# Optimization experiments

Measured on AMD Instinct MI355X. Metric: run time of the kernel, lower is better.

The kernel has to match this reference:

```python
import jax, jax.numpy as jnp
import numpy as np

B, S, H, N, L = 256, 64, 512, 16, 2
OUT_BITS = 32            # ceil(log2(n)), n = 2**32
PTR_BITS = 6             # ceil(log2(seq_len)), seq_len = 64
OUT_DIM = 3 + PTR_BITS   # = 9
T = 2 * OUT_BITS - 1     # 63 sequential decode steps


def _ln(x, g, b):
    m = jnp.mean(x, -1, keepdims=True)
    v = jnp.mean((x - m) ** 2, -1, keepdims=True)
    return (x - m) * jax.lax.rsqrt(v + 1e-5) * g + b


def _s4_step(A, Bm, Cm, D, oW, ob, s, x):
    # diagonal-SSM S4 block step: s (B,H,N) recurrent state, x (B,H) input
    s2 = A * s + Bm * x[:, :, None]
    y = jnp.einsum('bhn,hn->bh', s2, Cm) + D * x
    y = jax.nn.gelu(y, approximate=False) @ oW + ob
    return s2, y


def _forward(input_seq, in_W, in_b, A, Bm, Cm, D, outW, outb, ln_g, ln_b, head_W, head_b):
    Bsz = input_seq.shape[0]
    dt = input_seq.dtype
    x = input_seq @ in_W + in_b            # (B,S,H)
    encoded = x                            # encoded_inputs saved before S4 stack
    # ---- encoder: L S4 blocks, residual + layernorm ----
    for j in range(L):
        def step(s, xt, j=j):
            return _s4_step(A[j], Bm[j], Cm[j], D[j], outW[j], outb[j], s, xt)
        s0 = jnp.zeros((Bsz, H, N), dt)
        _, ys = jax.lax.scan(step, s0, jnp.swapaxes(x, 0, 1))
        x = _ln(jnp.swapaxes(ys, 0, 1) + x, ln_g[j], ln_b[j])
    dec0 = jnp.broadcast_to(jnp.array([0.0, 0.0, 1.0], dt), (Bsz, 3))
    carry0 = (jnp.zeros((L, Bsz, H, N), dt), jnp.zeros((Bsz, H), dt), dec0)
    ones1 = jnp.ones((Bsz, 1), dt)

    def dstep(carry, i):
        states, ctx, dec_in = carry
        dp = dec_in @ in_W + in_b          # (B,H)
        xd = dp
        new_states = []
        for j in range(L):
            s2, y = _s4_step(A[j], Bm[j], Cm[j], D[j], outW[j], outb[j], states[j], xd)
            new_states.append(s2)
            res = jnp.where(i == 0, dp, y)   # torch code: residual=proj on step 0, else doubles x_dec
            xd = _ln(y + res, ln_g[j], ln_b[j])
        is_out = (i % 2) == 0
        # pointer retrieval (only applied on odd steps via where)
        o_ptr = jax.nn.sigmoid((xd + ctx) @ head_W + head_b)
        ptr = jnp.argmax(o_ptr[:, 3:3 + PTR_BITS], axis=1)            # (B,)
        ptr_vec = jnp.take_along_axis(encoded, ptr[:, None, None], axis=1)[:, 0]
        ctx = jnp.where(is_out, ctx, ctx + ptr_vec)
        out = jax.nn.sigmoid((xd + ctx) @ head_W + head_b)            # (B,OUT_DIM)
        next_char = jnp.where(is_out, (out[:, 0:1] > 0.5).astype(dt), jnp.zeros((Bsz, 1), dt))
        tag0 = jnp.where(is_out, 1.0, 0.0) * ones1
        tag1 = ones1 - tag0
        dec_next = jnp.concatenate([next_char, tag0, tag1], axis=1)   # (B,3)
        return (jnp.stack(new_states), ctx, dec_next), out

    _, outs = jax.lax.scan(dstep, carry0, jnp.arange(T))
    return jnp.swapaxes(outs, 0, 1)        # (B, T, OUT_DIM)


def setup_inputs() -> dict:
    ks = jax.random.split(jax.random.key(0), 8)
    f32 = jnp.float32
    return {
        'input_seq': jax.random.uniform(ks[0], (B, S, 3), f32),
        'autoregressive_steps': T,
        'in_W': jax.random.normal(ks[1], (3, H), f32) * 0.5,
        'in_b': jnp.zeros((H,), f32),
        'A': jax.random.uniform(ks[2], (L, H, N), f32, 0.5, 0.99),
        'Bm': jax.random.normal(ks[3], (L, H, N), f32) * 0.1,
        'Cm': jax.random.normal(ks[4], (L, H, N), f32) * 0.1,
        'D': jnp.ones((L, H), f32),
        'outW': jax.random.normal(ks[5], (L, H, H), f32) * 0.02,
        'outb': jnp.zeros((L, H), f32),
        'ln_g': jnp.ones((L, H), f32),
        'ln_b': jnp.zeros((L, H), f32),
        'head_W': jax.random.normal(ks[6], (H, OUT_DIM), f32) * 0.05,
        'head_b': jnp.zeros((OUT_DIM,), f32),
    }


def reference(input_seq, autoregressive_steps, in_W, in_b, A, Bm, Cm, D, outW, outb, ln_g, ln_b, head_W, head_b):
    return _forward(input_seq, in_W, in_b, A, Bm, Cm, D, outW, outb, ln_g, ln_b, head_W, head_b)
```

## Files before the change

kernel.cpp:

```cpp
#include <hip/hip_runtime.h>
#include <math.h>

#define HDIM   512
#define NDIM   16
#define SEQ    64
#define TSTEPS 63
#define BATCH  256
#define ODIM   9
#define NTHR   512


__device__ __forceinline__ float gelu_f32(float x) {
    return 0.5f * x * (1.0f + erff(x * 0.70710678118654752440f));
}

__device__ __forceinline__ float sig32(float x) {
    return 1.0f / (1.0f + expf(-x));
}

__device__ __forceinline__ void load3_l2(const float* p0, const float* p1,
                                         const float* p2,
                                         float& v0, float& v1, float& v2) {
    asm volatile(
        "global_load_dword %0, %3, off sc0\n\t"
        "global_load_dword %1, %4, off sc0\n\t"
        "global_load_dword %2, %5, off sc0\n\t"
        "s_waitcnt vmcnt(0)"
        : "=&v"(v0), "=&v"(v1), "=&v"(v2)
        : "v"(p0), "v"(p1), "v"(p2)
        : "memory");
}
__device__ __forceinline__ float load1_l2(const float* p) {
    float v;
    asm volatile("global_load_dword %0, %1, off sc0\n\t"
                 "s_waitcnt vmcnt(0)"
                 : "=v"(v) : "v"(p) : "memory");
    return v;
}

__global__ __launch_bounds__(NTHR, 2)
void s4_decode_kernel(
    const float* __restrict__ input_seq,
    const float* __restrict__ in_W,
    const float* __restrict__ in_b,
    const float* __restrict__ Aarr,
    const float* __restrict__ Barr,
    const float* __restrict__ Carr,
    const float* __restrict__ Darr,
    const float* __restrict__ outW,
    const float* __restrict__ outb,
    const float* __restrict__ ln_g,
    const float* __restrict__ ln_b,
    const float* __restrict__ headW,
    const float* __restrict__ headb,
    float* __restrict__ out,
    float* gws, float* zws,
    unsigned* fg, unsigned* fz,
    unsigned* fx, unsigned* xid)
{
    __shared__ float  ld_xd[HDIM];
    __shared__ float  ld_gall[4 * HDIM];
    __shared__ float4 ld_z4[16 * 4 * 32];
    __shared__ float  ld_D0[HDIM];
    __shared__ float  ld_D1[HDIM];
    __shared__ float  ld_red[16];
    __shared__ float  ld_hred[8 * ODIM];
    __shared__ float  ld_logit[ODIM + 1];
    __shared__ float  ld_dec[4];
    __shared__ int    ld_ptr;
    __shared__ int    ld_fast;

    const int b    = blockIdx.x;
    const int tid  = threadIdx.x;
    const int hg   = tid >> 4;
    const int n    = tid & 15;
    const int mem  = (b >> 3) & 3;
    const int gbase = b - 8 * mem;
    const int c4   = tid & 31;
    const int rg   = tid >> 5;
    const int rgE  = (rg + ((b * 5) & 15)) & 15;
    const int base_row = rgE * 32;
    const int j0 = 0 + (0 >= mem), j1 = 1 + (1 >= mem), j2 = 2 + (2 >= mem);

    unsigned myxcd;
    asm volatile("s_getreg_b32 %0, hwreg(HW_REG_XCC_ID)" : "=s"(myxcd));
    if (tid == 0) {
        __hip_atomic_store(&xid[b], myxcd, __ATOMIC_RELAXED, __HIP_MEMORY_SCOPE_AGENT);
        __hip_atomic_store(&fx[b], 1u, __ATOMIC_RELEASE, __HIP_MEMORY_SCOPE_AGENT);
        unsigned ok = 1;
        #pragma unroll
        for (int j = 0; j < 4; ++j) {
            if (j == mem) continue;
            while (__hip_atomic_load(&fx[gbase + 8 * j],
                                     __ATOMIC_ACQUIRE, __HIP_MEMORY_SCOPE_AGENT) == 0)
                __builtin_amdgcn_s_sleep(1);
            ok &= (__hip_atomic_load(&xid[gbase + 8 * j],
                                     __ATOMIC_RELAXED, __HIP_MEMORY_SCOPE_AGENT) == myxcd);
        }
        ld_fast = (int)ok;
    }

    float s0[16], s1[16];
    float A0[16], B0[16], C0[16], A1[16], B1[16], C1[16];
    #pragma unroll
    for (int k = 0; k < 16; ++k) {
        int h  = hg + 32 * k;
        int i0 = h * NDIM + n;
        int i1 = (HDIM + h) * NDIM + n;
        A0[k] = Aarr[i0]; B0[k] = Barr[i0]; C0[k] = Carr[i0];
        A1[k] = Aarr[i1]; B1[k] = Barr[i1]; C1[k] = Carr[i1];
        s0[k] = 0.f; s1[k] = 0.f;
    }

    const float inb_t = in_b[tid];
    const float w0 = in_W[tid], w1 = in_W[HDIM + tid], w2 = in_W[2 * HDIM + tid];
    const float ob0 = outb[tid], ob1 = outb[HDIM + tid];
    const float lg0 = ln_g[tid], lg1 = ln_g[HDIM + tid];
    const float lb0 = ln_b[tid], lb1 = ln_b[HDIM + tid];

    ld_D0[tid] = Darr[tid];
    ld_D1[tid] = Darr[HDIM + tid];

    const float4* Wsl = (const float4*)outW + mem * 32 + c4;

    float ctxr = 0.f;
    if (tid == 0) { ld_dec[0] = 0.f; ld_dec[1] = 0.f; ld_dec[2] = 1.f; }
    __syncthreads();
    const bool fast = (ld_fast != 0);

    for (int i = 0; i < TSTEPS; ++i) {
        float dpv = fmaf(ld_dec[0], w0, fmaf(ld_dec[1], w1, fmaf(ld_dec[2], w2, inb_t)));
        __syncthreads();
        ld_xd[tid] = dpv;
        __syncthreads();

        #pragma unroll 1
        for (int blk = 0; blk < 2; ++blk) {
            const unsigned seq = (unsigned)(2 * i + blk + 1);
            {
                float* s  = blk ? s1 : s0;
                float* Ar = blk ? A1 : A0;
                float* Br = blk ? B1 : B0;
                float* Cr = blk ? C1 : C0;
                const float* Dl = blk ? ld_D1 : ld_D0;
                #pragma unroll
                for (int k = 0; k < 16; ++k) {
                    int h = hg + 32 * k;
                    float xh = ld_xd[h];
                    float sv = fmaf(Ar[k], s[k], Br[k] * xh);
                    s[k] = sv;
                    float p = sv * Cr[k];
                    p += __shfl_xor(p, 1);
                    p += __shfl_xor(p, 2);
                    p += __shfl_xor(p, 4);
                    p += __shfl_xor(p, 8);
                    if (n == 0) ld_gall[mem * HDIM + h] = gelu_f32(p + Dl[h] * xh);
                }
            }
            __syncthreads();
            if (fast) {
                gws[b * HDIM + tid] = ld_gall[mem * HDIM + tid];
            } else {
                __hip_atomic_store(&gws[b * HDIM + tid], ld_gall[mem * HDIM + tid],
                                   __ATOMIC_RELAXED, __HIP_MEMORY_SCOPE_AGENT);
            }
            __syncthreads();
            if (tid == 4)
                __hip_atomic_store(&fg[b], seq, __ATOMIC_RELAXED, __HIP_MEMORY_SCOPE_AGENT);
            if (tid < 3) {
                int j = tid + (tid >= mem ? 1 : 0);
                while (__hip_atomic_load(&fg[gbase + 8 * j],
                                         __ATOMIC_RELAXED, __HIP_MEMORY_SCOPE_AGENT) < seq)
                    __builtin_amdgcn_s_sleep(1);
            }
            __syncthreads();
            if (fast) {
                float v0, v1, v2;
                load3_l2(&gws[(gbase + 8 * j0) * HDIM + tid],
                         &gws[(gbase + 8 * j1) * HDIM + tid],
                         &gws[(gbase + 8 * j2) * HDIM + tid], v0, v1, v2);
                ld_gall[j0 * HDIM + tid] = v0;
                ld_gall[j1 * HDIM + tid] = v1;
                ld_gall[j2 * HDIM + tid] = v2;
            } else {
                ld_gall[j0 * HDIM + tid] =
                    __hip_atomic_load(&gws[(gbase + 8 * j0) * HDIM + tid],
                                      __ATOMIC_RELAXED, __HIP_MEMORY_SCOPE_AGENT);
                ld_gall[j1 * HDIM + tid] =
                    __hip_atomic_load(&gws[(gbase + 8 * j1) * HDIM + tid],
                                      __ATOMIC_RELAXED, __HIP_MEMORY_SCOPE_AGENT);
                ld_gall[j2 * HDIM + tid] =
                    __hip_atomic_load(&gws[(gbase + 8 * j2) * HDIM + tid],
                                      __ATOMIC_RELAXED, __HIP_MEMORY_SCOPE_AGENT);
            }
            __syncthreads();
            {
                const float4* Wb = Wsl + (size_t)blk * HDIM * 128;
                float4 acc[4];
                #pragma unroll
                for (int bi = 0; bi < 4; ++bi) acc[bi] = make_float4(0.f, 0.f, 0.f, 0.f);
                float4 a0 = Wb[(size_t)(base_row)     * 128];
                float4 a1 = Wb[(size_t)(base_row + 1) * 128];
                #pragma unroll 2
                for (int rr = 0; rr < 32; rr += 4) {
                    int rB = base_row + ((rr + 2) & 31);
                    float4 b0 = Wb[(size_t)rB * 128];
                    float4 b1 = Wb[(size_t)(rB + 1) * 128];
                    {
                        int r = base_row + rr;
                        #pragma unroll
                        for (int bi = 0; bi < 4; ++bi) {
                            float g0 = ld_gall[bi * HDIM + r];
                            float g1 = ld_gall[bi * HDIM + r + 1];
                            acc[bi].x = fmaf(g1, a1.x, fmaf(g0, a0.x, acc[bi].x));
                            acc[bi].y = fmaf(g1, a1.y, fmaf(g0, a0.y, acc[bi].y));
                            acc[bi].z = fmaf(g1, a1.z, fmaf(g0, a0.z, acc[bi].z));
                            acc[bi].w = fmaf(g1, a1.w, fmaf(g0, a0.w, acc[bi].w));
                        }
                    }
                    int rA = base_row + ((rr + 4) & 31);
                    a0 = Wb[(size_t)rA * 128];
                    a1 = Wb[(size_t)(rA + 1) * 128];
                    {
                        int r = base_row + rr + 2;
                        #pragma unroll
                        for (int bi = 0; bi < 4; ++bi) {
                            float g0 = ld_gall[bi * HDIM + r];
                            float g1 = ld_gall[bi * HDIM + r + 1];
                            acc[bi].x = fmaf(g1, b1.x, fmaf(g0, b0.x, acc[bi].x));
                            acc[bi].y = fmaf(g1, b1.y, fmaf(g0, b0.y, acc[bi].y));
                            acc[bi].z = fmaf(g1, b1.z, fmaf(g0, b0.z, acc[bi].z));
                            acc[bi].w = fmaf(g1, b1.w, fmaf(g0, b0.w, acc[bi].w));
                        }
                    }
                }
                #pragma unroll
                for (int bi = 0; bi < 4; ++bi)
                    ld_z4[(rg * 4 + bi) * 32 + c4] = acc[bi];
            }
            __syncthreads();
            {
                const float* zf = (const float*)ld_z4;
                int bi2 = tid >> 7;
                int col = tid & 127;
                float zv = 0.f;
                #pragma unroll
                for (int k = 0; k < 16; ++k) zv += zf[(k * 4 + bi2) * 128 + col];
                float* zp = &zws[(gbase + 8 * bi2) * HDIM + mem * 128 + col];
                if (fast) *zp = zv;
                else __hip_atomic_store(zp, zv, __ATOMIC_RELAXED, __HIP_MEMORY_SCOPE_AGENT);
            }
            __syncthreads();
            if (tid == 4)
                __hip_atomic_store(&fz[b], seq, __ATOMIC_RELAXED, __HIP_MEMORY_SCOPE_AGENT);
            if (tid < 3) {
                int j = tid + (tid >= mem ? 1 : 0);
                while (__hip_atomic_load(&fz[gbase + 8 * j],
                                         __ATOMIC_RELAXED, __HIP_MEMORY_SCOPE_AGENT) < seq)
                    __builtin_amdgcn_s_sleep(1);
            }
            __syncthreads();
            {
                float zraw = fast ? load1_l2(&zws[b * HDIM + tid])
                                  : __hip_atomic_load(&zws[b * HDIM + tid],
                                                      __ATOMIC_RELAXED,
                                                      __HIP_MEMORY_SCOPE_AGENT);
                float z = zraw + (blk ? ob1 : ob0);
                float res = (i == 0) ? dpv : z;
                float tmp = z + res;
                float v1 = tmp, v2 = tmp * tmp;
                #pragma unroll
                for (int m = 1; m < 64; m <<= 1) {
                    v1 += __shfl_xor(v1, m);
                    v2 += __shfl_xor(v2, m);
                }
                if ((tid & 63) == 0) {
                    ld_red[2 * (tid >> 6)]     = v1;
                    ld_red[2 * (tid >> 6) + 1] = v2;
                }
                __syncthreads();
                float s1r = 0.f, s2r = 0.f;
                #pragma unroll
                for (int q = 0; q < 8; ++q) { s1r += ld_red[2*q]; s2r += ld_red[2*q+1]; }
                float mu  = s1r * (1.f / 512.f);
                float var = s2r * (1.f / 512.f) - mu * mu;
                float rs  = rsqrtf(var + 1e-5f);
                __syncthreads();
                ld_xd[tid] = (tmp - mu) * rs * (blk ? lg1 : lg0) + (blk ? lb1 : lb0);
                __syncthreads();
            }
        }

        {
            float v = ld_xd[tid] + ctxr;
            const float* w = headW + tid * ODIM;
            float p[ODIM];
            #pragma unroll
            for (int o = 0; o < ODIM; ++o) p[o] = v * w[o];
            #pragma unroll
            for (int m = 1; m < 64; m <<= 1) {
                #pragma unroll
                for (int o = 0; o < ODIM; ++o) p[o] += __shfl_xor(p[o], m);
            }
            if ((tid & 63) == 0) {
                int wv = tid >> 6;
                #pragma unroll
                for (int o = 0; o < ODIM; ++o) ld_hred[wv * ODIM + o] = p[o];
            }
            __syncthreads();
            if (tid < ODIM) {
                float s = headb[tid];
                #pragma unroll
                for (int wv = 0; wv < 8; ++wv) s += ld_hred[wv * ODIM + tid];
                ld_logit[tid] = s;
            }
            __syncthreads();
        }

        const bool is_out = ((i & 1) == 0);
        if (is_out) {
            if (tid < ODIM)
                out[(b * TSTEPS + i) * ODIM + tid] = sig32(ld_logit[tid]);
            if (tid == 0) {
                float nc = (sig32(ld_logit[0]) > 0.5f) ? 1.f : 0.f;
                ld_dec[0] = nc; ld_dec[1] = 1.f; ld_dec[2] = 0.f;
            }
            __syncthreads();
        } else {
            if (tid == 0) {
                int best = 0; float bv = sig32(ld_logit[3]);
                #pragma unroll
                for (int o = 1; o < 6; ++o) {
                    float v2 = sig32(ld_logit[3 + o]);
                    if (v2 > bv) { bv = v2; best = o; }
                }
                ld_ptr = best;
                ld_dec[0] = 0.f; ld_dec[1] = 0.f; ld_dec[2] = 1.f;
            }
            __syncthreads();
            {
                const float* iseq = input_seq + (b * SEQ + ld_ptr) * 3;
                float e0 = iseq[0], e1 = iseq[1], e2 = iseq[2];
                ctxr += fmaf(e0, w0, fmaf(e1, w1, fmaf(e2, w2, inb_t)));
            }
            __syncthreads();
            {
                float v = ld_xd[tid] + ctxr;
                const float* w = headW + tid * ODIM;
                float p[ODIM];
                #pragma unroll
                for (int o = 0; o < ODIM; ++o) p[o] = v * w[o];
                #pragma unroll
                for (int m = 1; m < 64; m <<= 1) {
                    #pragma unroll
                    for (int o = 0; o < ODIM; ++o) p[o] += __shfl_xor(p[o], m);
                }
                if ((tid & 63) == 0) {
                    int wv = tid >> 6;
                    #pragma unroll
                    for (int o = 0; o < ODIM; ++o) ld_hred[wv * ODIM + o] = p[o];
                }
                __syncthreads();
                if (tid < ODIM) {
                    float s = headb[tid];
                    #pragma unroll
                    for (int wv = 0; wv < 8; ++wv) s += ld_hred[wv * ODIM + tid];
                    out[(b * TSTEPS + i) * ODIM + tid] = sig32(s);
                }
            }
            __syncthreads();
        }
    }
}

extern "C" void kernel_launch(void* const* d_in, const int* in_sizes, int n_in,
                              void* d_out, int out_size, void* d_ws, size_t ws_size,
                              hipStream_t stream) {
    (void)in_sizes; (void)n_in; (void)ws_size; (void)out_size;
    const float* input_seq = (const float*)d_in[0];
    const float* in_W   = (const float*)d_in[2];
    const float* in_b   = (const float*)d_in[3];
    const float* Aarr   = (const float*)d_in[4];
    const float* Barr   = (const float*)d_in[5];
    const float* Carr   = (const float*)d_in[6];
    const float* Darr   = (const float*)d_in[7];
    const float* outW   = (const float*)d_in[8];
    const float* outb   = (const float*)d_in[9];
    const float* ln_g   = (const float*)d_in[10];
    const float* ln_b   = (const float*)d_in[11];
    const float* headW  = (const float*)d_in[12];
    const float* headb  = (const float*)d_in[13];
    float* out = (float*)d_out;

    unsigned* fg  = (unsigned*)d_ws;
    unsigned* fz  = fg + BATCH;
    unsigned* fx  = fz + BATCH;
    unsigned* xid = fx + BATCH;
    float* gws = (float*)((char*)d_ws + 4096);
    float* zws = gws + BATCH * HDIM;

    hipMemsetAsync(d_ws, 0, 4096, stream);

    s4_decode_kernel<<<BATCH, NTHR, 0, stream>>>(
        input_seq, in_W, in_b, Aarr, Barr, Carr, Darr,
        outW, outb, ln_g, ln_b, headW, headb, out,
        gws, zws, fg, fz, fx, xid);
}
```

Before: 1.357 ms.

## Split hidden dim across 4-block groups so each block computes SSM for all 4 batches

Before, each block ran the full S4 recurrence for its own batch row and exchanged GELU outputs with the three peer blocks through global memory, then did a column-sliced matmul. Now each block owns a quarter of the hidden dimension for all four batch rows in its group. That removes the GELU exchange round (gws and fg flags) and leaves a single z-exchange per layer. The shuffle reduction is restructured as a transpose-style butterfly, the matmul uses float4 LDS reads with a 4-row prefetch, and head weights are cached in registers. The trade-offs are higher register pressure (launch bounds drop to 1 block per CU) and redundant layernorm and head work for all four rows in every block.

```diff
diff --git a/kernel.cpp b/kernel.cpp
--- a/kernel.cpp
+++ b/kernel.cpp
@@ -8,7 +8,11 @@
 #define BATCH  256
 #define ODIM   9
 #define NTHR   512
-
+#define GSTR   132
+#define SPIN_CAP (1 << 24)
+
+
+typedef float f32x4 __attribute__((ext_vector_type(4)));
 
 __device__ __forceinline__ float gelu_f32(float x) {
     return 0.5f * x * (1.0f + erff(x * 0.70710678118654752440f));
@@ -18,27 +22,30 @@
     return 1.0f / (1.0f + expf(-x));
 }
 
-__device__ __forceinline__ void load3_l2(const float* p0, const float* p1,
-                                         const float* p2,
-                                         float& v0, float& v1, float& v2) {
+__device__ __forceinline__ void load4x4_l2(const f32x4* p0, const f32x4* p1,
+                                           const f32x4* p2, const f32x4* p3,
+                                           f32x4& v0, f32x4& v1, f32x4& v2, f32x4& v3) {
     asm volatile(
-        "global_load_dword %0, %3, off sc0\n\t"
-        "global_load_dword %1, %4, off sc0\n\t"
-        "global_load_dword %2, %5, off sc0\n\t"
+        "global_load_dwordx4 %0, %4, off sc0\n\t"
+        "global_load_dwordx4 %1, %5, off sc0\n\t"
+        "global_load_dwordx4 %2, %6, off sc0\n\t"
+        "global_load_dwordx4 %3, %7, off sc0\n\t"
         "s_waitcnt vmcnt(0)"
-        : "=&v"(v0), "=&v"(v1), "=&v"(v2)
-        : "v"(p0), "v"(p1), "v"(p2)
+        : "=&v"(v0), "=&v"(v1), "=&v"(v2), "=&v"(v3)
+        : "v"(p0), "v"(p1), "v"(p2), "v"(p3)
         : "memory");
 }
-__device__ __forceinline__ float load1_l2(const float* p) {
-    float v;
-    asm volatile("global_load_dword %0, %1, off sc0\n\t"
-                 "s_waitcnt vmcnt(0)"
-                 : "=v"(v) : "v"(p) : "memory");
-    return v;
-}
-
-__global__ __launch_bounds__(NTHR, 2)
+
+__device__ __forceinline__ void fma_row4(float4& acc, const float4 g,
+                                         const float4 w0, const float4 w1,
+                                         const float4 w2, const float4 w3) {
+    acc.x = fmaf(g.w, w3.x, fmaf(g.z, w2.x, fmaf(g.y, w1.x, fmaf(g.x, w0.x, acc.x))));
+    acc.y = fmaf(g.w, w3.y, fmaf(g.z, w2.y, fmaf(g.y, w1.y, fmaf(g.x, w0.y, acc.y))));
+    acc.z = fmaf(g.w, w3.z, fmaf(g.z, w2.z, fmaf(g.y, w1.z, fmaf(g.x, w0.z, acc.z))));
+    acc.w = fmaf(g.w, w3.w, fmaf(g.z, w2.w, fmaf(g.y, w1.w, fmaf(g.x, w0.w, acc.w))));
+}
+
+__global__ __launch_bounds__(NTHR, 1)
 void s4_decode_kernel(
     const float* __restrict__ input_seq,
     const float* __restrict__ in_W,
@@ -54,33 +61,28 @@
     const float* __restrict__ headW,
     const float* __restrict__ headb,
     float* __restrict__ out,
-    float* gws, float* zws,
-    unsigned* fg, unsigned* fz,
+    float* zws,
+    unsigned* fz,
     unsigned* fx, unsigned* xid)
 {
-    __shared__ float  ld_xd[HDIM];
-    __shared__ float  ld_gall[4 * HDIM];
-    __shared__ float4 ld_z4[16 * 4 * 32];
-    __shared__ float  ld_D0[HDIM];
-    __shared__ float  ld_D1[HDIM];
-    __shared__ float  ld_red[16];
-    __shared__ float  ld_hred[8 * ODIM];
-    __shared__ float  ld_logit[ODIM + 1];
-    __shared__ float  ld_dec[4];
-    __shared__ int    ld_ptr;
+    __shared__ __align__(16) float  ld_x[4 * HDIM];
+    __shared__ __align__(16) float  ld_g[4 * GSTR];
+    __shared__ float4 ld_z4[16 * 128];
+    __shared__ float  ld_red[64];
+    __shared__ __align__(16) float  ld_hred[8 * 36];
+    __shared__ float  ld_logit[36];
+    __shared__ float  ld_dec[16];
+    __shared__ int    ld_ptr[4];
     __shared__ int    ld_fast;
 
-    const int b    = blockIdx.x;
-    const int tid  = threadIdx.x;
-    const int hg   = tid >> 4;
-    const int n    = tid & 15;
-    const int mem  = (b >> 3) & 3;
+    const int b     = blockIdx.x;
+    const int tid   = threadIdx.x;
+    const int n     = tid & 15;
+    const int hl32  = tid >> 4;
+    const int mem   = (b >> 3) & 3;
     const int gbase = b - 8 * mem;
-    const int c4   = tid & 31;
-    const int rg   = tid >> 5;
-    const int rgE  = (rg + ((b * 5) & 15)) & 15;
-    const int base_row = rgE * 32;
-    const int j0 = 0 + (0 >= mem), j1 = 1 + (1 >= mem), j2 = 2 + (2 >= mem);
+    const int hbase = 128 * mem;
+    const size_t zbase = (size_t)(((b >> 5) << 3) + (b & 7)) * (4 * HDIM * 4);
 
     unsigned myxcd;
     asm volatile("s_getreg_b32 %0, hwreg(HW_REG_XCC_ID)" : "=s"(myxcd));
@@ -91,9 +93,12 @@
         #pragma unroll
         for (int j = 0; j < 4; ++j) {
             if (j == mem) continue;
+            int guard = 0;
             while (__hip_atomic_load(&fx[gbase + 8 * j],
-                                     __ATOMIC_ACQUIRE, __HIP_MEMORY_SCOPE_AGENT) == 0)
+                                     __ATOMIC_ACQUIRE, __HIP_MEMORY_SCOPE_AGENT) == 0) {
                 __builtin_amdgcn_s_sleep(1);
+                if (++guard > SPIN_CAP) { ok = 0; break; }
+            }
             ok &= (__hip_atomic_load(&xid[gbase + 8 * j],
                                      __ATOMIC_RELAXED, __HIP_MEMORY_SCOPE_AGENT) == myxcd);
         }
@@ -101,217 +106,273 @@
     }
 
     float s0[16], s1[16];
-    float A0[16], B0[16], C0[16], A1[16], B1[16], C1[16];
+    float A0[4], B0[4], C0[4], A1[4], B1[4], C1[4], Dm0[4], Dm1[4];
     #pragma unroll
-    for (int k = 0; k < 16; ++k) {
-        int h  = hg + 32 * k;
-        int i0 = h * NDIM + n;
-        int i1 = (HDIM + h) * NDIM + n;
+    for (int k = 0; k < 4; ++k) {
+        const int h  = hbase + hl32 + 32 * k;
+        const int i0 = h * NDIM + n;
+        const int i1 = (HDIM + h) * NDIM + n;
         A0[k] = Aarr[i0]; B0[k] = Barr[i0]; C0[k] = Carr[i0];
         A1[k] = Aarr[i1]; B1[k] = Barr[i1]; C1[k] = Carr[i1];
-        s0[k] = 0.f; s1[k] = 0.f;
+        Dm0[k] = (n == 0) ? Darr[h] : 0.f;
+        Dm1[k] = (n == 0) ? Darr[HDIM + h] : 0.f;
     }
+    #pragma unroll
+    for (int v = 0; v < 16; ++v) { s0[v] = 0.f; s1[v] = 0.f; }
 
     const float inb_t = in_b[tid];
     const float w0 = in_W[tid], w1 = in_W[HDIM + tid], w2 = in_W[2 * HDIM + tid];
     const float ob0 = outb[tid], ob1 = outb[HDIM + tid];
     const float lg0 = ln_g[tid], lg1 = ln_g[HDIM + tid];
     const float lb0 = ln_b[tid], lb1 = ln_b[HDIM + tid];
-
-    ld_D0[tid] = Darr[tid];
-    ld_D1[tid] = Darr[HDIM + tid];
-
-    const float4* Wsl = (const float4*)outW + mem * 32 + c4;
-
-    float ctxr = 0.f;
-    if (tid == 0) { ld_dec[0] = 0.f; ld_dec[1] = 0.f; ld_dec[2] = 1.f; }
+    float hw[ODIM];
+    #pragma unroll
+    for (int o = 0; o < ODIM; ++o) hw[o] = headW[tid * ODIM + o];
+
+    float ctx[4] = {0.f, 0.f, 0.f, 0.f};
+    if (tid < 4) { ld_dec[4 * tid] = 0.f; ld_dec[4 * tid + 1] = 0.f; ld_dec[4 * tid + 2] = 1.f; }
     __syncthreads();
     const bool fast = (ld_fast != 0);
 
     for (int i = 0; i < TSTEPS; ++i) {
-        float dpv = fmaf(ld_dec[0], w0, fmaf(ld_dec[1], w1, fmaf(ld_dec[2], w2, inb_t)));
+        float dpr[4];
+        #pragma unroll
+        for (int j = 0; j < 4; ++j) {
+            dpr[j] = fmaf(ld_dec[4 * j], w0,
+                     fmaf(ld_dec[4 * j + 1], w1,
+                     fmaf(ld_dec[4 * j + 2], w2, inb_t)));
+            ld_x[j * HDIM + tid] = dpr[j];
+        }
         __syncthreads();
-        ld_xd[tid] = dpv;
-        __syncthreads();
-
-        #pragma unroll 1
+
+        float xn[4];
+
+        #pragma unroll
         for (int blk = 0; blk < 2; ++blk) {
             const unsigned seq = (unsigned)(2 * i + blk + 1);
-            {
-                float* s  = blk ? s1 : s0;
-                float* Ar = blk ? A1 : A0;
-                float* Br = blk ? B1 : B0;
-                float* Cr = blk ? C1 : C0;
-                const float* Dl = blk ? ld_D1 : ld_D0;
-                #pragma unroll
-                for (int k = 0; k < 16; ++k) {
-                    int h = hg + 32 * k;
-                    float xh = ld_xd[h];
-                    float sv = fmaf(Ar[k], s[k], Br[k] * xh);
-                    s[k] = sv;
-                    float p = sv * Cr[k];
-                    p += __shfl_xor(p, 1);
-                    p += __shfl_xor(p, 2);
-                    p += __shfl_xor(p, 4);
-                    p += __shfl_xor(p, 8);
-                    if (n == 0) ld_gall[mem * HDIM + h] = gelu_f32(p + Dl[h] * xh);
-                }
-            }
-            __syncthreads();
-            if (fast) {
-                gws[b * HDIM + tid] = ld_gall[mem * HDIM + tid];
-            } else {
-                __hip_atomic_store(&gws[b * HDIM + tid], ld_gall[mem * HDIM + tid],
-                                   __ATOMIC_RELAXED, __HIP_MEMORY_SCOPE_AGENT);
-            }
-            __syncthreads();
-            if (tid == 4)
-                __hip_atomic_store(&fg[b], seq, __ATOMIC_RELAXED, __HIP_MEMORY_SCOPE_AGENT);
-            if (tid < 3) {
-                int j = tid + (tid >= mem ? 1 : 0);
-                while (__hip_atomic_load(&fg[gbase + 8 * j],
-                                         __ATOMIC_RELAXED, __HIP_MEMORY_SCOPE_AGENT) < seq)
-                    __builtin_amdgcn_s_sleep(1);
-            }
-            __syncthreads();
-            if (fast) {
-                float v0, v1, v2;
-                load3_l2(&gws[(gbase + 8 * j0) * HDIM + tid],
-                         &gws[(gbase + 8 * j1) * HDIM + tid],
-                         &gws[(gbase + 8 * j2) * HDIM + tid], v0, v1, v2);
-                ld_gall[j0 * HDIM + tid] = v0;
-                ld_gall[j1 * HDIM + tid] = v1;
-                ld_gall[j2 * HDIM + tid] = v2;
-            } else {
-                ld_gall[j0 * HDIM + tid] =
-                    __hip_atomic_load(&gws[(gbase + 8 * j0) * HDIM + tid],
-                                      __ATOMIC_RELAXED, __HIP_MEMORY_SCOPE_AGENT);
-                ld_gall[j1 * HDIM + tid] =
-                    __hip_atomic_load(&gws[(gbase + 8 * j1) * HDIM + tid],
-                                      __ATOMIC_RELAXED, __HIP_MEMORY_SCOPE_AGENT);
-                ld_gall[j2 * HDIM + tid] =
-                    __hip_atomic_load(&gws[(gbase + 8 * j2) * HDIM + tid],
-                                      __ATOMIC_RELAXED, __HIP_MEMORY_SCOPE_AGENT);
-            }
-            __syncthreads();
-            {
-                const float4* Wb = Wsl + (size_t)blk * HDIM * 128;
-                float4 acc[4];
-                #pragma unroll
-                for (int bi = 0; bi < 4; ++bi) acc[bi] = make_float4(0.f, 0.f, 0.f, 0.f);
-                float4 a0 = Wb[(size_t)(base_row)     * 128];
-                float4 a1 = Wb[(size_t)(base_row + 1) * 128];
-                #pragma unroll 2
-                for (int rr = 0; rr < 32; rr += 4) {
-                    int rB = base_row + ((rr + 2) & 31);
-                    float4 b0 = Wb[(size_t)rB * 128];
-                    float4 b1 = Wb[(size_t)(rB + 1) * 128];
-                    {
-                        int r = base_row + rr;
-                        #pragma unroll
-                        for (int bi = 0; bi < 4; ++bi) {
-                            float g0 = ld_gall[bi * HDIM + r];
-                            float g1 = ld_gall[bi * HDIM + r + 1];
-                            acc[bi].x = fmaf(g1, a1.x, fmaf(g0, a0.x, acc[bi].x));
-                            acc[bi].y = fmaf(g1, a1.y, fmaf(g0, a0.y, acc[bi].y));
-                            acc[bi].z = fmaf(g1, a1.z, fmaf(g0, a0.z, acc[bi].z));
-                            acc[bi].w = fmaf(g1, a1.w, fmaf(g0, a0.w, acc[bi].w));
-                        }
-                    }
-                    int rA = base_row + ((rr + 4) & 31);
-                    a0 = Wb[(size_t)rA * 128];
-                    a1 = Wb[(size_t)(rA + 1) * 128];
-                    {
-                        int r = base_row + rr + 2;
-                        #pragma unroll
-                        for (int bi = 0; bi < 4; ++bi) {
-                            float g0 = ld_gall[bi * HDIM + r];
-                            float g1 = ld_gall[bi * HDIM + r + 1];
-                            acc[bi].x = fmaf(g1, b1.x, fmaf(g0, b0.x, acc[bi].x));
-                            acc[bi].y = fmaf(g1, b1.y, fmaf(g0, b0.y, acc[bi].y));
-                            acc[bi].z = fmaf(g1, b1.z, fmaf(g0, b0.z, acc[bi].z));
-                            acc[bi].w = fmaf(g1, b1.w, fmaf(g0, b0.w, acc[bi].w));
-                        }
-                    }
-                }
-                #pragma unroll
-                for (int bi = 0; bi < 4; ++bi)
-                    ld_z4[(rg * 4 + bi) * 32 + c4] = acc[bi];
-            }
-            __syncthreads();
-            {
-                const float* zf = (const float*)ld_z4;
-                int bi2 = tid >> 7;
-                int col = tid & 127;
-                float zv = 0.f;
-                #pragma unroll
-                for (int k = 0; k < 16; ++k) zv += zf[(k * 4 + bi2) * 128 + col];
-                float* zp = &zws[(gbase + 8 * bi2) * HDIM + mem * 128 + col];
-                if (fast) *zp = zv;
-                else __hip_atomic_store(zp, zv, __ATOMIC_RELAXED, __HIP_MEMORY_SCOPE_AGENT);
+
+            float p[16];
+            {
+                float*       sp = blk ? s1 : s0;
+                const float* Ar = blk ? A1 : A0;
+                const float* Br = blk ? B1 : B0;
+                const float* Cr = blk ? C1 : C0;
+                const float* Dm = blk ? Dm1 : Dm0;
+                #pragma unroll
+                for (int j = 0; j < 4; ++j)
+                    #pragma unroll
+                    for (int k = 0; k < 4; ++k) {
+                        const int v = j * 4 + k;
+                        const float x  = ld_x[j * HDIM + hbase + hl32 + 32 * k];
+                        const float sv = fmaf(Ar[k], sp[v], Br[k] * x);
+                        sp[v] = sv;
+                        p[v] = fmaf(Dm[k], x, sv * Cr[k]);
+                    }
+            }
+            {
+                float q8[8];
+                { const bool bt = (n & 1) != 0;
+                  #pragma unroll
+                  for (int u = 0; u < 8; ++u) {
+                      const float sd = bt ? p[2 * u] : p[2 * u + 1];
+                      const float rc = __shfl_xor(sd, 1);
+                      q8[u] = (bt ? p[2 * u + 1] : p[2 * u]) + rc;
+                  } }
+                float q4[4];
+                { const bool bt = (n & 2) != 0;
+                  #pragma unroll
+                  for (int u = 0; u < 4; ++u) {
+                      const float sd = bt ? q8[2 * u] : q8[2 * u + 1];
+                      const float rc = __shfl_xor(sd, 2);
+                      q4[u] = (bt ? q8[2 * u + 1] : q8[2 * u]) + rc;
+                  } }
+                float q2[2];
+                { const bool bt = (n & 4) != 0;
+                  #pragma unroll
+                  for (int u = 0; u < 2; ++u) {
+                      const float sd = bt ? q4[2 * u] : q4[2 * u + 1];
+                      const float rc = __shfl_xor(sd, 4);
+                      q2[u] = (bt ? q4[2 * u + 1] : q4[2 * u]) + rc;
+                  } }
+                float y;
+                { const bool bt = (n & 8) != 0;
+                  const float sd = bt ? q2[0] : q2[1];
+                  const float rc = __shfl_xor(sd, 8);
+                  y = (bt ? q2[1] : q2[0]) + rc; }
+                ld_g[(n >> 2) * GSTR + hl32 + 32 * (n & 3)] = gelu_f32(y);
+            }
+            __syncthreads();
+
+            {
+                const int rg   = tid >> 7;
+                const int c    = tid & 127;
+                const int rge  = (rg + b) & 3;
+                const int rb32 = rge * 32;
+                const int roff = (b & 7) * 4;
+                const float4* Wb = (const float4*)outW
+                    + (((size_t)blk) << 16) + (size_t)(hbase + rb32) * 128 + c;
+                float4 acc0 = make_float4(0.f, 0.f, 0.f, 0.f);
+                float4 acc1 = acc0, acc2 = acc0, acc3 = acc0;
+                int r = roff;
+                float4 cw0 = Wb[(size_t)(r + 0) * 128], cw1 = Wb[(size_t)(r + 1) * 128],
+                       cw2 = Wb[(size_t)(r + 2) * 128], cw3 = Wb[(size_t)(r + 3) * 128];
+                #pragma unroll
+                for (int ch = 0; ch < 8; ++ch) {
+                    float4 nw0, nw1, nw2, nw3;
+                    const int rn = (roff + 4 * ch + 4) & 31;
+                    if (ch < 7) {
+                        nw0 = Wb[(size_t)(rn + 0) * 128]; nw1 = Wb[(size_t)(rn + 1) * 128];
+                        nw2 = Wb[(size_t)(rn + 2) * 128]; nw3 = Wb[(size_t)(rn + 3) * 128];
+                    }
+                    const float4 g0 = *(const float4*)&ld_g[0 * GSTR + rb32 + r];
+                    const float4 g1 = *(const float4*)&ld_g[1 * GSTR + rb32 + r];
+                    const float4 g2 = *(const float4*)&ld_g[2 * GSTR + rb32 + r];
+                    const float4 g3 = *(const float4*)&ld_g[3 * GSTR + rb32 + r];
+                    fma_row4(acc0, g0, cw0, cw1, cw2, cw3);
+                    fma_row4(acc1, g1, cw0, cw1, cw2, cw3);
+                    fma_row4(acc2, g2, cw0, cw1, cw2, cw3);
+                    fma_row4(acc3, g3, cw0, cw1, cw2, cw3);
+                    if (ch < 7) { cw0 = nw0; cw1 = nw1; cw2 = nw2; cw3 = nw3; r = rn; }
+                }
+                ld_z4[(rg * 4 + 0) * 128 + c] = acc0;
+                ld_z4[(rg * 4 + 1) * 128 + c] = acc1;
+                ld_z4[(rg * 4 + 2) * 128 + c] = acc2;
+                ld_z4[(rg * 4 + 3) * 128 + c] = acc3;
+            }
+            __syncthreads();
+
+            {
+                const int b2 = tid >> 7;
+                const int c  = tid & 127;
+                const float4 z0 = ld_z4[(0 * 4 + b2) * 128 + c];
+                const float4 z1 = ld_z4[(1 * 4 + b2) * 128 + c];
+                const float4 z2 = ld_z4[(2 * 4 + b2) * 128 + c];
+                const float4 z3 = ld_z4[(3 * 4 + b2) * 128 + c];
+                const float sx = ((z0.x + z1.x) + z2.x) + z3.x;
+                const float sy = ((z0.y + z1.y) + z2.y) + z3.y;
+                const float sz = ((z0.z + z1.z) + z2.z) + z3.z;
+                const float sw = ((z0.w + z1.w) + z2.w) + z3.w;
+                float* zp = zws + zbase + (size_t)(b2 * HDIM + 4 * c) * 4 + mem;
+                if (fast) {
+                    zp[0] = sx; zp[4] = sy; zp[8] = sz; zp[12] = sw;
+                } else {
+                    __hip_atomic_store(zp + 0,  sx, __ATOMIC_RELAXED, __HIP_MEMORY_SCOPE_AGENT);
+                    __hip_atomic_store(zp + 4,  sy, __ATOMIC_RELAXED, __HIP_MEMORY_SCOPE_AGENT);
+                    __hip_atomic_store(zp + 8,  sz, __ATOMIC_RELAXED, __HIP_MEMORY_SCOPE_AGENT);
+                    __hip_atomic_store(zp + 12, sw, __ATOMIC_RELAXED, __HIP_MEMORY_SCOPE_AGENT);
+                }
             }
             __syncthreads();
             if (tid == 4)
                 __hip_atomic_store(&fz[b], seq, __ATOMIC_RELAXED, __HIP_MEMORY_SCOPE_AGENT);
             if (tid < 3) {
-                int j = tid + (tid >= mem ? 1 : 0);
+                const int j = tid + (tid >= mem ? 1 : 0);
+                int guard = 0;
                 while (__hip_atomic_load(&fz[gbase + 8 * j],
-                                         __ATOMIC_RELAXED, __HIP_MEMORY_SCOPE_AGENT) < seq)
+                                         __ATOMIC_RELAXED, __HIP_MEMORY_SCOPE_AGENT) < seq) {
                     __builtin_amdgcn_s_sleep(1);
-            }
-            __syncthreads();
-            {
-                float zraw = fast ? load1_l2(&zws[b * HDIM + tid])
-                                  : __hip_atomic_load(&zws[b * HDIM + tid],
-                                                      __ATOMIC_RELAXED,
-                                                      __HIP_MEMORY_SCOPE_AGENT);
-                float z = zraw + (blk ? ob1 : ob0);
-                float res = (i == 0) ? dpv : z;
-                float tmp = z + res;
-                float v1 = tmp, v2 = tmp * tmp;
+                    if (++guard > SPIN_CAP) break;
+                }
+            }
+            __syncthreads();
+
+            float z[4];
+            {
+                const float ob = blk ? ob1 : ob0;
+                if (fast) {
+                    const f32x4* zq = (const f32x4*)(zws + zbase);
+                    f32x4 m0, m1, m2, m3;
+                    load4x4_l2(zq + 0 * HDIM + tid, zq + 1 * HDIM + tid,
+                               zq + 2 * HDIM + tid, zq + 3 * HDIM + tid, m0, m1, m2, m3);
+                    z[0] = (((m0.x + m0.y) + m0.z) + m0.w) + ob;
+                    z[1] = (((m1.x + m1.y) + m1.z) + m1.w) + ob;
+                    z[2] = (((m2.x + m2.y) + m2.z) + m2.w) + ob;
+                    z[3] = (((m3.x + m3.y) + m3.z) + m3.w) + ob;
+                } else {
+                    #pragma unroll
+                    for (int j = 0; j < 4; ++j) {
+                        const float* zf = zws + zbase + (size_t)(j * HDIM + tid) * 4;
+                        const float a0 = __hip_atomic_load(zf + 0, __ATOMIC_RELAXED, __HIP_MEMORY_SCOPE_AGENT);
+                        const float a1 = __hip_atomic_load(zf + 1, __ATOMIC_RELAXED, __HIP_MEMORY_SCOPE_AGENT);
+                        const float a2 = __hip_atomic_load(zf + 2, __ATOMIC_RELAXED, __HIP_MEMORY_SCOPE_AGENT);
+                        const float a3 = __hip_atomic_load(zf + 3, __ATOMIC_RELAXED, __HIP_MEMORY_SCOPE_AGENT);
+                        z[j] = (((a0 + a1) + a2) + a3) + ob;
+                    }
+                }
+            }
+
+            {
+                float tmp[4], v1[4], v2[4];
+                #pragma unroll
+                for (int j = 0; j < 4; ++j) {
+                    const float res = (i == 0) ? dpr[j] : z[j];
+                    tmp[j] = z[j] + res;
+                    v1[j] = tmp[j];
+                    v2[j] = tmp[j] * tmp[j];
+                }
                 #pragma unroll
                 for (int m = 1; m < 64; m <<= 1) {
-                    v1 += __shfl_xor(v1, m);
-                    v2 += __shfl_xor(v2, m);
+                    #pragma unroll
+                    for (int j = 0; j < 4; ++j) {
+                        v1[j] += __shfl_xor(v1[j], m);
+                        v2[j] += __shfl_xor(v2[j], m);
+                    }
                 }
                 if ((tid & 63) == 0) {
-                    ld_red[2 * (tid >> 6)]     = v1;
-                    ld_red[2 * (tid >> 6) + 1] = v2;
+                    const int wv = tid >> 6;
+                    #pragma unroll
+                    for (int j = 0; j < 4; ++j) {
+                        ld_red[wv * 8 + 2 * j]     = v1[j];
+                        ld_red[wv * 8 + 2 * j + 1] = v2[j];
+                    }
                 }
                 __syncthreads();
-                float s1r = 0.f, s2r = 0.f;
-                #pragma unroll
-                for (int q = 0; q < 8; ++q) { s1r += ld_red[2*q]; s2r += ld_red[2*q+1]; }
-                float mu  = s1r * (1.f / 512.f);
-                float var = s2r * (1.f / 512.f) - mu * mu;
-                float rs  = rsqrtf(var + 1e-5f);
-                __syncthreads();
-                ld_xd[tid] = (tmp - mu) * rs * (blk ? lg1 : lg0) + (blk ? lb1 : lb0);
-                __syncthreads();
+                const float glG = blk ? lg1 : lg0;
+                const float glB = blk ? lb1 : lb0;
+                #pragma unroll
+                for (int j = 0; j < 4; ++j) {
+                    float s1r = 0.f, s2r = 0.f;
+                    #pragma unroll
+                    for (int q = 0; q < 8; ++q) {
+                        s1r += ld_red[q * 8 + 2 * j];
+                        s2r += ld_red[q * 8 + 2 * j + 1];
+                    }
+                    const float mu  = s1r * (1.f / 512.f);
+                    const float var = s2r * (1.f / 512.f) - mu * mu;
+                    const float rs  = rsqrtf(var + 1e-5f);
+                    xn[j] = (tmp[j] - mu) * rs * glG + glB;
+                }
+                if (blk == 0) {
+                    #pragma unroll
+                    for (int j = 0; j < 4; ++j) ld_x[j * HDIM + tid] = xn[j];
+                    __syncthreads();
+                }
             }
         }
 
         {
-            float v = ld_xd[tid] + ctxr;
-            const float* w = headW + tid * ODIM;
-            float p[ODIM];
+            float hp[36];
             #pragma unroll
-            for (int o = 0; o < ODIM; ++o) p[o] = v * w[o];
+            for (int j = 0; j < 4; ++j) {
+                const float v = xn[j] + ctx[j];
+                #pragma unroll
+                for (int o = 0; o < ODIM; ++o) hp[j * ODIM + o] = v * hw[o];
+            }
             #pragma unroll
-            for (int m = 1; m < 64; m <<= 1) {
-                #pragma unroll
-                for (int o = 0; o < ODIM; ++o) p[o] += __shfl_xor(p[o], m);
-            }
+            for (int m = 1; m < 64; m <<= 1)
+                #pragma unroll
+                for (int u = 0; u < 36; ++u) hp[u] += __shfl_xor(hp[u], m);
             if ((tid & 63) == 0) {
-                int wv = tid >> 6;
-                #pragma unroll
-                for (int o = 0; o < ODIM; ++o) ld_hred[wv * ODIM + o] = p[o];
-            }
-            __syncthreads();
-            if (tid < ODIM) {
-                float s = headb[tid];
-                #pragma unroll
-                for (int wv = 0; wv < 8; ++wv) s += ld_hred[wv * ODIM + tid];
+                float4* hd = (float4*)&ld_hred[(tid >> 6) * 36];
+                #pragma unroll
+                for (int u = 0; u < 9; ++u)
+                    hd[u] = make_float4(hp[4 * u], hp[4 * u + 1], hp[4 * u + 2], hp[4 * u + 3]);
+            }
+            __syncthreads();
+            if (tid < 36) {
+                float s = headb[tid % ODIM];
+                #pragma unroll
+                for (int q = 0; q < 8; ++q) s += ld_hred[q * 36 + tid];
                 ld_logit[tid] = s;
             }
             __syncthreads();
@@ -320,55 +381,57 @@
         const bool is_out = ((i & 1) == 0);
         if (is_out) {
             if (tid < ODIM)
-                out[(b * TSTEPS + i) * ODIM + tid] = sig32(ld_logit[tid]);
-            if (tid == 0) {
-                float nc = (sig32(ld_logit[0]) > 0.5f) ? 1.f : 0.f;
-                ld_dec[0] = nc; ld_dec[1] = 1.f; ld_dec[2] = 0.f;
+                out[((size_t)b * TSTEPS + i) * ODIM + tid] = sig32(ld_logit[mem * ODIM + tid]);
+            if (tid < 4) {
+                const float nc = (sig32(ld_logit[tid * ODIM]) > 0.5f) ? 1.f : 0.f;
+                ld_dec[4 * tid] = nc; ld_dec[4 * tid + 1] = 1.f; ld_dec[4 * tid + 2] = 0.f;
             }
             __syncthreads();
         } else {
-            if (tid == 0) {
-                int best = 0; float bv = sig32(ld_logit[3]);
+            if (tid < 4) {
+                const int base9 = tid * ODIM;
+                int best = 0; float bv = sig32(ld_logit[base9 + 3]);
                 #pragma unroll
                 for (int o = 1; o < 6; ++o) {
-                    float v2 = sig32(ld_logit[3 + o]);
+                    const float v2 = sig32(ld_logit[base9 + 3 + o]);
                     if (v2 > bv) { bv = v2; best = o; }
                 }
-                ld_ptr = best;
-                ld_dec[0] = 0.f; ld_dec[1] = 0.f; ld_dec[2] = 1.f;
-            }
-            __syncthreads();
-            {
-                const float* iseq = input_seq + (b * SEQ + ld_ptr) * 3;
-                float e0 = iseq[0], e1 = iseq[1], e2 = iseq[2];
-                ctxr += fmaf(e0, w0, fmaf(e1, w1, fmaf(e2, w2, inb_t)));
-            }
-            __syncthreads();
-            {
-                float v = ld_xd[tid] + ctxr;
-                const float* w = headW + tid * ODIM;
-                float p[ODIM];
-                #pragma unroll
-                for (int o = 0; o < ODIM; ++o) p[o] = v * w[o];
-                #pragma unroll
-                for (int m = 1; m < 64; m <<= 1) {
-                    #pragma unroll
-                    for (int o = 0; o < ODIM; ++o) p[o] += __shfl_xor(p[o], m);
-                }
+                ld_ptr[tid] = best;
+                ld_dec[4 * tid] = 0.f; ld_dec[4 * tid + 1] = 0.f; ld_dec[4 * tid + 2] = 1.f;
+            }
+            __syncthreads();
+            #pragma unroll
+            for (int j = 0; j < 4; ++j) {
+                const float* iseq = input_seq + ((size_t)(gbase + 8 * j) * SEQ + ld_ptr[j]) * 3;
+                ctx[j] += fmaf(iseq[0], w0, fmaf(iseq[1], w1, fmaf(iseq[2], w2, inb_t)));
+            }
+            {
+                float hq[36];
+                #pragma unroll
+                for (int j = 0; j < 4; ++j) {
+                    const float v = xn[j] + ctx[j];
+                    #pragma unroll
+                    for (int o = 0; o < ODIM; ++o) hq[j * ODIM + o] = v * hw[o];
+                }
+                #pragma unroll
+                for (int m = 1; m < 64; m <<= 1)
+                    #pragma unroll
+                    for (int u = 0; u < 36; ++u) hq[u] += __shfl_xor(hq[u], m);
                 if ((tid & 63) == 0) {
-                    int wv = tid >> 6;
-                    #pragma unroll
-                    for (int o = 0; o < ODIM; ++o) ld_hred[wv * ODIM + o] = p[o];
+                    float4* hd = (float4*)&ld_hred[(tid >> 6) * 36];
+                    #pragma unroll
+                    for (int u = 0; u < 9; ++u)
+                        hd[u] = make_float4(hq[4 * u], hq[4 * u + 1], hq[4 * u + 2], hq[4 * u + 3]);
                 }
                 __syncthreads();
                 if (tid < ODIM) {
                     float s = headb[tid];
                     #pragma unroll
-                    for (int wv = 0; wv < 8; ++wv) s += ld_hred[wv * ODIM + tid];
-                    out[(b * TSTEPS + i) * ODIM + tid] = sig32(s);
-                }
-            }
-            __syncthreads();
+                    for (int q = 0; q < 8; ++q) s += ld_hred[q * 36 + mem * ODIM + tid];
+                    out[((size_t)b * TSTEPS + i) * ODIM + tid] = sig32(s);
+                }
+                __syncthreads();
+            }
         }
     }
 }
@@ -392,17 +455,15 @@
     const float* headb  = (const float*)d_in[13];
     float* out = (float*)d_out;
 
-    unsigned* fg  = (unsigned*)d_ws;
-    unsigned* fz  = fg + BATCH;
-    unsigned* fx  = fz + BATCH;
-    unsigned* xid = fx + BATCH;
-    float* gws = (float*)((char*)d_ws + 4096);
-    float* zws = gws + BATCH * HDIM;
+    unsigned* fz  = (unsigned*)d_ws + BATCH;
+    unsigned* fx  = (unsigned*)d_ws + 2 * BATCH;
+    unsigned* xid = (unsigned*)d_ws + 3 * BATCH;
+    float* zws = (float*)((char*)d_ws + 4096);
 
     hipMemsetAsync(d_ws, 0, 4096, stream);
 
     s4_decode_kernel<<<BATCH, NTHR, 0, stream>>>(
         input_seq, in_W, in_b, Aarr, Barr, Carr, Darr,
         outW, outb, ln_g, ln_b, headW, headb, out,
-        gws, zws, fg, fz, fx, xid);
-}
+        zws, fz, fx, xid);
+}
```

New measurement: 2.906 ms. 114% more time.
